# Optimization experiments

Measured on AMD Instinct MI355X. Metric: run time of the kernel, lower is better.

## Reference

```python
import jax, jax.numpy as jnp
import numpy as np

N_EMBD = 1024
BLOCK_SIZE = 2048
B = 8
LN_EPS = 1e-5


def _mlp(x, W1, b1, W2, b2):
    # Linear -> exact GELU -> Linear (torch nn.GELU default is erf-based)
    h = jax.nn.gelu(x @ W1 + b1, approximate=False)
    return h @ W2 + b2


def setup_inputs() -> dict:
    key = jax.random.key(0)
    ks = jax.random.split(key, 14)
    C = N_EMBD
    std = 0.02
    d = {"x": jax.random.normal(ks[0], (B, BLOCK_SIZE, C), dtype=jnp.float32)}
    names = ["q", "k", "v"]
    i = 1
    for n in names:
        d[f"W1{n}"] = jax.random.normal(ks[i], (C, C), dtype=jnp.float32) * std; i += 1
        d[f"b1{n}"] = jnp.zeros((C,), dtype=jnp.float32)
        d[f"W2{n}"] = jax.random.normal(ks[i], (C, C), dtype=jnp.float32) * std; i += 1
        d[f"b2{n}"] = jnp.zeros((C,), dtype=jnp.float32)
    d["ln_w"] = jnp.ones((C,), dtype=jnp.float32)
    d["ln_b"] = jnp.zeros((C,), dtype=jnp.float32)
    return d


def reference(x, W1q, b1q, W2q, b2q, W1k, b1k, W2k, b2k, W1v, b1v, W2v, b2v, ln_w, ln_b):
    Bsz, T, C = x.shape
    q = _mlp(x, W1q, b1q, W2q, b2q)
    k = _mlp(x, W1k, b1k, W2k, b2k)
    v = _mlp(x, W1v, b1v, W2v, b2v)
    scale = np.sqrt(N_EMBD * BLOCK_SIZE).astype(np.float32)
    scores = jnp.einsum("bid,bjd->bij", q, k) / scale  # [B,T,T]
    mask = jnp.tril(jnp.ones((T, T), dtype=scores.dtype))
    scores = scores * mask
    out = jnp.einsum("bij,bjd->bid", scores, v)  # [B,T,C]
    # LayerNorm with weight+bias, eps=1e-5
    mu = jnp.mean(out, axis=-1, keepdims=True)
    var = jnp.mean(jnp.square(out - mu), axis=-1, keepdims=True)
    out = (out - mu) * jax.lax.rsqrt(var + LN_EPS) * ln_w + ln_b
    return out
```

## Files before the change

kernel.cpp:

```cpp
#include <hip/hip_runtime.h>
#include <math.h>

#define BM 128
#define BN 128
#define BK 64

typedef _Float16 f16x8 __attribute__((ext_vector_type(8)));
typedef __attribute__((ext_vector_type(4))) float f32x4;

typedef const __attribute__((address_space(1))) void* gas_ptr;
typedef __attribute__((address_space(3))) void* las_ptr;

enum { OP_NONE = 0, OP_BIAS_GELU = 1, OP_BIAS = 2, OP_SCALE_MASK = 3 };

__device__ __forceinline__ unsigned short f2h(float f) {
    _Float16 h = (_Float16)f;
    unsigned short u;
    __builtin_memcpy(&u, &h, 2);
    return u;
}
__device__ __forceinline__ float h2f(unsigned short u) {
    _Float16 h;
    __builtin_memcpy(&h, &u, 2);
    return (float)h;
}

__device__ __forceinline__ float fast_gelu(float x) {
    float x2 = x * x;
    float p  = x * (-1.5957691216f - 0.0713548164f * x2);
    float t  = __expf(p);
    return x * __builtin_amdgcn_rcpf(1.0f + t);
}

template <int EPI, bool CAUSAL_K, bool TRI, bool REVM>
__global__ __launch_bounds__(256, 4) void gemm_bt(
    const unsigned short* __restrict__ A,
    const unsigned short* __restrict__ BT,
    unsigned short* __restrict__ Cw,
    const float* __restrict__ bias0,
    const float* __restrict__ bias1,
    const float* __restrict__ bias2,
    int M, int N, int K,
    long long sA, long long sB, long long sC,
    float scale)
{
    __shared__ __align__(16) unsigned short As[BM * BK];
    __shared__ __align__(16) unsigned short Bs[BN * BK];

    const int tid  = threadIdx.x;
    const int wave = tid >> 6;
    const int lane = tid & 63;

    int bm, bn, z;
    if (TRI) {
        const int t = blockIdx.x;
        int i = (int)((sqrtf(8.0f * t + 1.0f) - 1.0f) * 0.5f);
        while ((i + 1) * (i + 2) / 2 <= t) i++;
        while (i * (i + 1) / 2 > t) i--;
        const int j = t - i * (i + 1) / 2;
        bm = i * BM;
        bn = j * BN;
        z  = blockIdx.y;
    } else {
        bm = (REVM ? (gridDim.x - 1 - blockIdx.x) : blockIdx.x) * BM;
        bn = blockIdx.y * BN;
        z  = blockIdx.z;
    }

    const unsigned short* Ab = A  + (long long)z * sA;
    const unsigned short* Bb = BT + (long long)z * sB;
    unsigned short*       Cb = Cw + (long long)z * sC;
    const float* bias = nullptr;
    if (EPI == OP_BIAS || EPI == OP_BIAS_GELU)
        bias = (z == 0) ? bias0 : (z == 1) ? bias1 : bias2;

    const int wm = (wave >> 1) * 64;
    const int wn = (wave & 1) * 64;

    f32x4 acc[4][4];
    #pragma unroll
    for (int i = 0; i < 4; i++)
        #pragma unroll
        for (int j = 0; j < 4; j++)
            acc[i][j] = (f32x4){0.f, 0.f, 0.f, 0.f};

    int Keff = K;
    if (CAUSAL_K) {
        int kl = bm + BM;
        Keff = kl < K ? kl : K;
    }

    const int srow = lane >> 3;
    const int gchw = ((lane & 7) ^ (srow & 7)) * 8;
    const int fr   = lane & 15;
    const int quad = lane >> 4;

    const unsigned short* pA = Ab + (long long)(bm + wave * 32 + srow) * K + gchw;
    const unsigned short* pB = Bb + (long long)(bn + wave * 32 + srow) * K + gchw;
    const long long rstep = 8ll * K;

    for (int k0 = 0; k0 < Keff; k0 += BK) {
        #pragma unroll
        for (int s = 0; s < 4; ++s) {
            const int t = wave * 4 + s;
            __builtin_amdgcn_global_load_lds((gas_ptr)(const void*)(pA + s * rstep),
                                             (las_ptr)(void*)&As[t * 512 + lane * 8],
                                             16, 0, 0);
            __builtin_amdgcn_global_load_lds((gas_ptr)(const void*)(pB + s * rstep),
                                             (las_ptr)(void*)&Bs[t * 512 + lane * 8],
                                             16, 0, 0);
        }
        pA += BK;
        pB += BK;
        __syncthreads();

        #pragma unroll
        for (int kk = 0; kk < 2; ++kk) {
            f16x8 fa[4], fb[4];
            #pragma unroll
            for (int i = 0; i < 4; i++) {
                const int row  = wm + i * 16 + fr;
                const int slot = row * 8 + ((kk * 4 + quad) ^ (fr & 7));
                fa[i] = *(const f16x8*)&As[slot * 8];
            }
            #pragma unroll
            for (int j = 0; j < 4; j++) {
                const int row  = wn + j * 16 + fr;
                const int slot = row * 8 + ((kk * 4 + quad) ^ (fr & 7));
                fb[j] = *(const f16x8*)&Bs[slot * 8];
            }
            #pragma unroll
            for (int i = 0; i < 4; i++)
                #pragma unroll
                for (int j = 0; j < 4; j++)
                    acc[i][j] = __builtin_amdgcn_mfma_f32_16x16x32_f16(
                        fa[i], fb[j], acc[i][j], 0, 0, 0);
        }
        __syncthreads();
    }

    const int er = quad;
    const int ec = fr;
    float bj[4];
    if (EPI == OP_BIAS || EPI == OP_BIAS_GELU) {
        #pragma unroll
        for (int j = 0; j < 4; j++) bj[j] = bias[bn + wn + j * 16 + ec];
    }
    #pragma unroll
    for (int i = 0; i < 4; i++) {
        #pragma unroll
        for (int r = 0; r < 4; r++) {
            const int row = bm + wm + i * 16 + er * 4 + r;
            #pragma unroll
            for (int j = 0; j < 4; j++) {
                const int col = bn + wn + j * 16 + ec;
                float v = acc[i][j][r];
                if (EPI == OP_BIAS_GELU) {
                    v = fast_gelu(v + bj[j]);
                } else if (EPI == OP_BIAS) {
                    v += bj[j];
                } else if (EPI == OP_SCALE_MASK) {
                    v *= scale;
                    if (col > row) v = 0.f;
                }
                Cb[(long long)row * N + col] = f2h(v);
            }
        }
    }
}

__global__ __launch_bounds__(256) void cvt_f32_f16(
    const float4* __restrict__ in, ushort4* __restrict__ out)
{
    int i = blockIdx.x * 256 + threadIdx.x;
    float4 f = in[i];
    ushort4 o;
    o.x = f2h(f.x); o.y = f2h(f.y); o.z = f2h(f.z); o.w = f2h(f.w);
    out[i] = o;
}

__global__ __launch_bounds__(256) void wprep(
    const float* __restrict__ s0, const float* __restrict__ s1,
    const float* __restrict__ s2, const float* __restrict__ s3,
    const float* __restrict__ s4, const float* __restrict__ s5,
    unsigned short* __restrict__ W1T, unsigned short* __restrict__ W2T)
{
    const int C = 1024;
    const int z = blockIdx.z;
    const float* in = (z == 0) ? s0 : (z == 1) ? s1 : (z == 2) ? s2
                    : (z == 3) ? s3 : (z == 4) ? s4 : s5;
    unsigned short* out = (z < 3) ? (W1T + (long long)z * C * C)
                                  : (W2T + (long long)(z - 3) * C * C);
    __shared__ unsigned short tile[32][33];
    const int bx = blockIdx.x * 32;
    const int by = blockIdx.y * 32;
    const int x = threadIdx.x;
    for (int y = threadIdx.y; y < 32; y += 8)
        tile[y][x] = f2h(in[(long long)(by + y) * C + (bx + x)]);
    __syncthreads();
    for (int y = threadIdx.y; y < 32; y += 8)
        out[(long long)(bx + y) * C + (by + x)] = tile[x][y];
}

__global__ __launch_bounds__(256) void transpose64_f16(
    const unsigned short* __restrict__ in,
    unsigned short* __restrict__ out,
    int rows, int cols,
    long long sIn, long long sOut)
{
    __shared__ unsigned short tile[64][68];
    const unsigned short* ip = in  + (long long)blockIdx.z * sIn;
    unsigned short*       op = out + (long long)blockIdx.z * sOut;
    const int bx = blockIdx.x * 64;
    const int by = blockIdx.y * 64;
    const int tid = threadIdx.x;
    const int rsub = tid >> 4;
    const int c4   = (tid & 15) * 4;
    #pragma unroll
    for (int it = 0; it < 4; it++) {
        const int r = it * 16 + rsub;
        ushort4 v = *(const ushort4*)&ip[(long long)(by + r) * cols + (bx + c4)];
        tile[r][c4]     = v.x;
        tile[r][c4 + 1] = v.y;
        tile[r][c4 + 2] = v.z;
        tile[r][c4 + 3] = v.w;
    }
    __syncthreads();
    #pragma unroll
    for (int it = 0; it < 4; it++) {
        const int cc = it * 16 + rsub;
        ushort4 v;
        v.x = tile[c4][cc];
        v.y = tile[c4 + 1][cc];
        v.z = tile[c4 + 2][cc];
        v.w = tile[c4 + 3][cc];
        *(ushort4*)&op[(long long)(bx + cc) * rows + (by + c4)] = v;
    }
}

__global__ __launch_bounds__(256) void layernorm_h(
    const unsigned short* __restrict__ X,
    const float* __restrict__ W,
    const float* __restrict__ Bv,
    float* __restrict__ Y)
{
    const int row = blockIdx.x;
    const int tid = threadIdx.x;
    ushort4 u = ((const ushort4*)(X + (long long)row * 1024))[tid];
    float f0 = h2f(u.x), f1 = h2f(u.y), f2 = h2f(u.z), f3 = h2f(u.w);
    float s  = f0 + f1 + f2 + f3;
    float ss = f0 * f0 + f1 * f1 + f2 * f2 + f3 * f3;
    #pragma unroll
    for (int off = 32; off > 0; off >>= 1) {
        s  += __shfl_down(s, off);
        ss += __shfl_down(ss, off);
    }
    __shared__ float red[2][4];
    const int wv = tid >> 6;
    if ((tid & 63) == 0) { red[0][wv] = s; red[1][wv] = ss; }
    __syncthreads();
    float S  = red[0][0] + red[0][1] + red[0][2] + red[0][3];
    float SS = red[1][0] + red[1][1] + red[1][2] + red[1][3];
    float mu  = S * (1.f / 1024.f);
    float var = SS * (1.f / 1024.f) - mu * mu;
    float rs  = rsqrtf(var + 1e-5f);
    float4 w4 = ((const float4*)W)[tid];
    float4 b4 = ((const float4*)Bv)[tid];
    float4 o;
    o.x = (f0 - mu) * rs * w4.x + b4.x;
    o.y = (f1 - mu) * rs * w4.y + b4.y;
    o.z = (f2 - mu) * rs * w4.z + b4.z;
    o.w = (f3 - mu) * rs * w4.w + b4.w;
    ((float4*)(Y + (long long)row * 1024))[tid] = o;
}

extern "C" void kernel_launch(void* const* d_in, const int* in_sizes, int n_in,
                              void* d_out, int out_size, void* d_ws, size_t ws_size,
                              hipStream_t stream)
{
    const int C  = 1024;
    const int T  = 2048;
    const int NB = 8;
    const int MT = NB * T;

    const float* x = (const float*)d_in[0];
    const float* W1q = (const float*)d_in[1];
    const float* b1q = (const float*)d_in[2];
    const float* W2q = (const float*)d_in[3];
    const float* b2q = (const float*)d_in[4];
    const float* W1k = (const float*)d_in[5];
    const float* b1k = (const float*)d_in[6];
    const float* W2k = (const float*)d_in[7];
    const float* b2k = (const float*)d_in[8];
    const float* W1v = (const float*)d_in[9];
    const float* b1v = (const float*)d_in[10];
    const float* W2v = (const float*)d_in[11];
    const float* b2v = (const float*)d_in[12];
    const float* lnw = (const float*)d_in[13];
    const float* lnb = (const float*)d_in[14];

    char* wsp = (char*)d_ws;
    auto take = [&](size_t bytes) {
        char* p = wsp;
        wsp += (bytes + 255) & ~(size_t)255;
        return p;
    };

    const size_t MATE = (size_t)MT * C;

    unsigned short* W1T  = (unsigned short*)take((size_t)3 * C * C * 2);
    unsigned short* W2T  = (unsigned short*)take((size_t)3 * C * C * 2);
    unsigned short* xb   = (unsigned short*)take(MATE * 2);
    unsigned short* qkv  = (unsigned short*)take(3 * MATE * 2);
    unsigned short* hreg = (unsigned short*)take(3 * MATE * 2);
    unsigned short* qb   = qkv;
    unsigned short* kb   = qkv + MATE;
    unsigned short* vb   = qkv + 2 * MATE;
    unsigned short* vT   = xb;
    unsigned short* scb  = hreg;
    unsigned short* opre = hreg + (size_t)NB * T * T;

    cvt_f32_f16<<<dim3(MT * C / 1024, 1, 1), dim3(256, 1, 1), 0, stream>>>(
        (const float4*)x, (ushort4*)xb);

    wprep<<<dim3(C / 32, C / 32, 6), dim3(32, 8, 1), 0, stream>>>(
        W1q, W1k, W1v, W2q, W2k, W2v, W1T, W2T);

    dim3 blk(256, 1, 1);

    gemm_bt<OP_BIAS_GELU, false, false, false><<<dim3(MT / BM, C / BN, 3), blk, 0, stream>>>(
        xb, W1T, hreg, b1q, b1k, b1v, MT, C, C,
        0, (long long)C * C, (long long)MATE, 1.f);

    gemm_bt<OP_BIAS, false, false, false><<<dim3(MT / BM, C / BN, 3), blk, 0, stream>>>(
        hreg, W2T, qkv, b2q, b2k, b2v, MT, C, C,
        (long long)MATE, (long long)C * C, (long long)MATE, 1.f);

    transpose64_f16<<<dim3(C / 64, T / 64, NB), blk, 0, stream>>>(
        vb, vT, T, C, (long long)T * C, (long long)T * C);

    float inv_scale = 1.0f / sqrtf((float)C * (float)T);
    gemm_bt<OP_SCALE_MASK, false, true, false><<<dim3(136, NB, 1), blk, 0, stream>>>(
        qb, kb, scb, nullptr, nullptr, nullptr, T, T, C,
        (long long)T * C, (long long)T * C, (long long)T * T, inv_scale);

    gemm_bt<OP_NONE, true, false, true><<<dim3(T / BM, C / BN, NB), blk, 0, stream>>>(
        scb, vT, opre, nullptr, nullptr, nullptr, T, C, T,
        (long long)T * T, (long long)T * C, (long long)T * C, 1.f);

    layernorm_h<<<dim3(MT, 1, 1), dim3(256, 1, 1), 0, stream>>>(
        opre, lnw, lnb, (float*)d_out);
}
```

Measured before the change: 538.8 us.

## Pair causal row tiles in scores@V GEMM, widen weight transpose, wave-per-row layernorm

Adds a gemm_pair kernel for scores@V in which each block computes two row tiles, one from the top and its mirror from the bottom. Because the causal K range grows with row index, every block gets a balanced amount of work, and the block count is halved. The weight transpose moves to 64x64 tiles with float4 loads. LayerNorm now uses one wave per row with xor shuffles instead of a block-wide shared-memory reduction. The gemm_pair launch bounds of (256,4) may constrain registers, and the paired block runs its two tiles one after the other.

```diff
diff --git a/kernel.cpp b/kernel.cpp
--- a/kernel.cpp
+++ b/kernel.cpp
@@ -169,6 +169,111 @@
     }
 }
 
+__global__ __launch_bounds__(256, 4) void gemm_pair(
+    const unsigned short* __restrict__ A,
+    const unsigned short* __restrict__ BT,
+    unsigned short* __restrict__ Cw,
+    int M, int N, int K,
+    long long sA, long long sB, long long sC)
+{
+    __shared__ __align__(16) unsigned short As[BM * BK];
+    __shared__ __align__(16) unsigned short Bs[BN * BK];
+
+    const int tid  = threadIdx.x;
+    const int wave = tid >> 6;
+    const int lane = tid & 63;
+
+    const int wm = (wave >> 1) * 64;
+    const int wn = (wave & 1) * 64;
+
+    const int srow = lane >> 3;
+    const int gchw = ((lane & 7) ^ (srow & 7)) * 8;
+    const int fr   = lane & 15;
+    const int quad = lane >> 4;
+
+    const int z  = blockIdx.z;
+    const int bn = blockIdx.y * BN;
+    const unsigned short* Ab = A  + (long long)z * sA;
+    const unsigned short* Bb = BT + (long long)z * sB;
+    unsigned short*       Cb = Cw + (long long)z * sC;
+
+    #pragma unroll 1
+    for (int half = 0; half < 2; ++half) {
+        const int mb = half ? (2 * (int)gridDim.x - 1 - (int)blockIdx.x)
+                            : (int)blockIdx.x;
+        const int bm = mb * BM;
+
+        f32x4 acc[4][4];
+        #pragma unroll
+        for (int i = 0; i < 4; i++)
+            #pragma unroll
+            for (int j = 0; j < 4; j++)
+                acc[i][j] = (f32x4){0.f, 0.f, 0.f, 0.f};
+
+        int Keff = bm + BM;
+        if (Keff > K) Keff = K;
+
+        const unsigned short* pA = Ab + (long long)(bm + wave * 32 + srow) * K + gchw;
+        const unsigned short* pB = Bb + (long long)(bn + wave * 32 + srow) * K + gchw;
+        const long long rstep = 8ll * K;
+
+        for (int k0 = 0; k0 < Keff; k0 += BK) {
+            #pragma unroll
+            for (int s = 0; s < 4; ++s) {
+                const int t = wave * 4 + s;
+                __builtin_amdgcn_global_load_lds((gas_ptr)(const void*)(pA + s * rstep),
+                                                 (las_ptr)(void*)&As[t * 512 + lane * 8],
+                                                 16, 0, 0);
+                __builtin_amdgcn_global_load_lds((gas_ptr)(const void*)(pB + s * rstep),
+                                                 (las_ptr)(void*)&Bs[t * 512 + lane * 8],
+                                                 16, 0, 0);
+            }
+            pA += BK;
+            pB += BK;
+            __syncthreads();
+
+            #pragma unroll
+            for (int kk = 0; kk < 2; ++kk) {
+                f16x8 fa[4], fb[4];
+                #pragma unroll
+                for (int i = 0; i < 4; i++) {
+                    const int row  = wm + i * 16 + fr;
+                    const int slot = row * 8 + ((kk * 4 + quad) ^ (fr & 7));
+                    fa[i] = *(const f16x8*)&As[slot * 8];
+                }
+                #pragma unroll
+                for (int j = 0; j < 4; j++) {
+                    const int row  = wn + j * 16 + fr;
+                    const int slot = row * 8 + ((kk * 4 + quad) ^ (fr & 7));
+                    fb[j] = *(const f16x8*)&Bs[slot * 8];
+                }
+                #pragma unroll
+                for (int i = 0; i < 4; i++)
+                    #pragma unroll
+                    for (int j = 0; j < 4; j++)
+                        acc[i][j] = __builtin_amdgcn_mfma_f32_16x16x32_f16(
+                            fa[i], fb[j], acc[i][j], 0, 0, 0);
+            }
+            __syncthreads();
+        }
+
+        const int er = quad;
+        const int ec = fr;
+        #pragma unroll
+        for (int i = 0; i < 4; i++) {
+            #pragma unroll
+            for (int r = 0; r < 4; r++) {
+                const int row = bm + wm + i * 16 + er * 4 + r;
+                #pragma unroll
+                for (int j = 0; j < 4; j++) {
+                    const int col = bn + wn + j * 16 + ec;
+                    Cb[(long long)row * N + col] = f2h(acc[i][j][r]);
+                }
+            }
+        }
+    }
+}
+
 __global__ __launch_bounds__(256) void cvt_f32_f16(
     const float4* __restrict__ in, ushort4* __restrict__ out)
 {
@@ -179,7 +284,7 @@
     out[i] = o;
 }
 
-__global__ __launch_bounds__(256) void wprep(
+__global__ __launch_bounds__(256) void wprep64(
     const float* __restrict__ s0, const float* __restrict__ s1,
     const float* __restrict__ s2, const float* __restrict__ s3,
     const float* __restrict__ s4, const float* __restrict__ s5,
@@ -191,15 +296,32 @@
                     : (z == 3) ? s3 : (z == 4) ? s4 : s5;
     unsigned short* out = (z < 3) ? (W1T + (long long)z * C * C)
                                   : (W2T + (long long)(z - 3) * C * C);
-    __shared__ unsigned short tile[32][33];
-    const int bx = blockIdx.x * 32;
-    const int by = blockIdx.y * 32;
-    const int x = threadIdx.x;
-    for (int y = threadIdx.y; y < 32; y += 8)
-        tile[y][x] = f2h(in[(long long)(by + y) * C + (bx + x)]);
+    __shared__ unsigned short tile[64][68];
+    const int bx = blockIdx.x * 64;
+    const int by = blockIdx.y * 64;
+    const int tid = threadIdx.x;
+    const int rsub = tid >> 4;
+    const int c4   = (tid & 15) * 4;
+    #pragma unroll
+    for (int it = 0; it < 4; it++) {
+        const int r = it * 16 + rsub;
+        float4 v = *(const float4*)&in[(long long)(by + r) * C + (bx + c4)];
+        tile[r][c4]     = f2h(v.x);
+        tile[r][c4 + 1] = f2h(v.y);
+        tile[r][c4 + 2] = f2h(v.z);
+        tile[r][c4 + 3] = f2h(v.w);
+    }
     __syncthreads();
-    for (int y = threadIdx.y; y < 32; y += 8)
-        out[(long long)(bx + y) * C + (by + x)] = tile[x][y];
+    #pragma unroll
+    for (int it = 0; it < 4; it++) {
+        const int cc = it * 16 + rsub;
+        ushort4 v;
+        v.x = tile[c4][cc];
+        v.y = tile[c4 + 1][cc];
+        v.z = tile[c4 + 2][cc];
+        v.w = tile[c4 + 3][cc];
+        *(ushort4*)&out[(long long)(bx + cc) * C + (by + c4)] = v;
+    }
 }
 
 __global__ __launch_bounds__(256) void transpose64_f16(
@@ -238,40 +360,45 @@
     }
 }
 
-__global__ __launch_bounds__(256) void layernorm_h(
+__global__ __launch_bounds__(256) void layernorm_w(
     const unsigned short* __restrict__ X,
     const float* __restrict__ W,
     const float* __restrict__ Bv,
     float* __restrict__ Y)
 {
-    const int row = blockIdx.x;
-    const int tid = threadIdx.x;
-    ushort4 u = ((const ushort4*)(X + (long long)row * 1024))[tid];
-    float f0 = h2f(u.x), f1 = h2f(u.y), f2 = h2f(u.z), f3 = h2f(u.w);
-    float s  = f0 + f1 + f2 + f3;
-    float ss = f0 * f0 + f1 * f1 + f2 * f2 + f3 * f3;
-    #pragma unroll
-    for (int off = 32; off > 0; off >>= 1) {
-        s  += __shfl_down(s, off);
-        ss += __shfl_down(ss, off);
-    }
-    __shared__ float red[2][4];
-    const int wv = tid >> 6;
-    if ((tid & 63) == 0) { red[0][wv] = s; red[1][wv] = ss; }
-    __syncthreads();
-    float S  = red[0][0] + red[0][1] + red[0][2] + red[0][3];
-    float SS = red[1][0] + red[1][1] + red[1][2] + red[1][3];
-    float mu  = S * (1.f / 1024.f);
-    float var = SS * (1.f / 1024.f) - mu * mu;
-    float rs  = rsqrtf(var + 1e-5f);
-    float4 w4 = ((const float4*)W)[tid];
-    float4 b4 = ((const float4*)Bv)[tid];
-    float4 o;
-    o.x = (f0 - mu) * rs * w4.x + b4.x;
-    o.y = (f1 - mu) * rs * w4.y + b4.y;
-    o.z = (f2 - mu) * rs * w4.z + b4.z;
-    o.w = (f3 - mu) * rs * w4.w + b4.w;
-    ((float4*)(Y + (long long)row * 1024))[tid] = o;
+    const int wave = threadIdx.x >> 6;
+    const int lane = threadIdx.x & 63;
+    const long long row = (long long)blockIdx.x * 4 + wave;
+    const unsigned short* xr = X + row * 1024;
+    float f[16];
+    float s = 0.f, ss = 0.f;
+    #pragma unroll
+    for (int t = 0; t < 4; t++) {
+        ushort4 u = *(const ushort4*)&xr[lane * 4 + t * 256];
+        float a = h2f(u.x), b = h2f(u.y), c = h2f(u.z), d = h2f(u.w);
+        f[t * 4 + 0] = a; f[t * 4 + 1] = b; f[t * 4 + 2] = c; f[t * 4 + 3] = d;
+        s  += a + b + c + d;
+        ss += a * a + b * b + c * c + d * d;
+    }
+    #pragma unroll
+    for (int off = 32; off >= 1; off >>= 1) {
+        s  += __shfl_xor(s, off);
+        ss += __shfl_xor(ss, off);
+    }
+    const float mu  = s * (1.f / 1024.f);
+    const float var = ss * (1.f / 1024.f) - mu * mu;
+    const float rs  = rsqrtf(var + 1e-5f);
+    #pragma unroll
+    for (int t = 0; t < 4; t++) {
+        float4 w4 = *(const float4*)&W[lane * 4 + t * 256];
+        float4 b4 = *(const float4*)&Bv[lane * 4 + t * 256];
+        float4 o;
+        o.x = (f[t * 4 + 0] - mu) * rs * w4.x + b4.x;
+        o.y = (f[t * 4 + 1] - mu) * rs * w4.y + b4.y;
+        o.z = (f[t * 4 + 2] - mu) * rs * w4.z + b4.z;
+        o.w = (f[t * 4 + 3] - mu) * rs * w4.w + b4.w;
+        *(float4*)&Y[row * 1024 + lane * 4 + t * 256] = o;
+    }
 }
 
 extern "C" void kernel_launch(void* const* d_in, const int* in_sizes, int n_in,
@@ -323,7 +450,7 @@
     cvt_f32_f16<<<dim3(MT * C / 1024, 1, 1), dim3(256, 1, 1), 0, stream>>>(
         (const float4*)x, (ushort4*)xb);
 
-    wprep<<<dim3(C / 32, C / 32, 6), dim3(32, 8, 1), 0, stream>>>(
+    wprep64<<<dim3(C / 64, C / 64, 6), dim3(256, 1, 1), 0, stream>>>(
         W1q, W1k, W1v, W2q, W2k, W2v, W1T, W2T);
 
     dim3 blk(256, 1, 1);
@@ -344,10 +471,10 @@
         qb, kb, scb, nullptr, nullptr, nullptr, T, T, C,
         (long long)T * C, (long long)T * C, (long long)T * T, inv_scale);
 
-    gemm_bt<OP_NONE, true, false, true><<<dim3(T / BM, C / BN, NB), blk, 0, stream>>>(
-        scb, vT, opre, nullptr, nullptr, nullptr, T, C, T,
-        (long long)T * T, (long long)T * C, (long long)T * C, 1.f);
-
-    layernorm_h<<<dim3(MT, 1, 1), dim3(256, 1, 1), 0, stream>>>(
+    gemm_pair<<<dim3(T / BM / 2, C / BN, NB), blk, 0, stream>>>(
+        scb, vT, opre, T, C, T,
+        (long long)T * T, (long long)T * C, (long long)T * C);
+
+    layernorm_w<<<dim3(MT / 4, 1, 1), dim3(256, 1, 1), 0, stream>>>(
         opre, lnw, lnb, (float*)d_out);
 }
```

Measured after the change: 523.2 us. 2.9% less time.
